# Kernel optimization log

Hardware: AMD Instinct MI355X
Metric: run time of the kernel (lower is better)

Reference implementation:

```python
import jax, jax.numpy as jnp
import numpy as np

B, S, E, NH = 2, 2048, 512, 4
DH = E // NH  # 128
KSZ = 4      # causal conv kernel size


def setup_inputs() -> dict:
    key = jax.random.key(0)
    ks = jax.random.split(key, 12)
    hw_std = (2.0 / 5.0 / DH) ** 0.5
    return {
        "x": jax.random.normal(ks[0], (B, S, E), jnp.float32),
        "W_up": jax.random.normal(ks[1], (2 * E, E), jnp.float32) * 0.02,
        "Wq": jax.random.normal(ks[2], (NH, DH, DH), jnp.float32) * hw_std,
        "Wk": jax.random.normal(ks[3], (NH, DH, DH), jnp.float32) * hw_std,
        "Wv": jax.random.normal(ks[4], (NH, DH, DH), jnp.float32) * hw_std,
        "conv_w": jax.random.normal(ks[5], (E, E, KSZ), jnp.float32) * (1.0 / (E * KSZ) ** 0.5),
        "conv_b": jnp.zeros((E,), jnp.float32),
        "Wi": jax.random.normal(ks[6], (NH, 3 * E), jnp.float32) * 0.01,
        "bi": jax.random.normal(ks[7], (NH,), jnp.float32) * 0.1,
        "Wf": jax.random.normal(ks[8], (NH, 3 * E), jnp.float32) * 0.01,
        "bf": jax.random.normal(ks[9], (NH,), jnp.float32),
        "skip": jnp.ones((E,), jnp.float32),
        "W_down": jax.random.normal(ks[10], (E, E), jnp.float32) * 0.02,
        "b_down": jnp.zeros((E,), jnp.float32),
    }


def _headwise(u, W):
    # LinearHeadwiseExpand: x -> [B,S,NH,dh] @ [NH,od,dh]
    b, s, e = u.shape
    nh = W.shape[0]
    uh = u.reshape(b, s, nh, -1)
    return jnp.einsum('bshd,hod->bsho', uh, W).reshape(b, s, e)


def reference(x, W_up, Wq, Wk, Wv, conv_w, conv_b, Wi, bi, Wf, bf, skip, W_down, b_down):
    b, s, e = x.shape
    nh = Wq.shape[0]
    dh = e // nh
    eps = 1e-6

    x_inner = x @ W_up.T                        # [B,S,2E]
    x_mlstm, z = jnp.split(x_inner, 2, axis=-1)

    # causal conv1d: left-pad kernel_size-1, trim implicit via padding spec
    xc = jnp.transpose(x_mlstm, (0, 2, 1))      # [B,E,S]
    conv = jax.lax.conv_general_dilated(
        xc, conv_w, window_strides=(1,), padding=[(KSZ - 1, 0)],
        dimension_numbers=('NCH', 'OIH', 'NCH')) + conv_b[None, :, None]
    x_conv_act = jax.nn.silu(jnp.transpose(conv, (0, 2, 1)))  # [B,S,E]

    q = _headwise(x_conv_act, Wq)
    k = _headwise(x_conv_act, Wk)
    v = _headwise(x_mlstm, Wv)

    gate_in = jnp.concatenate([q, k, v], axis=-1)           # [B,S,3E]
    igate = jnp.transpose(gate_in @ Wi.T + bi, (0, 2, 1))   # [B,NH,S]
    fgate = jnp.transpose(gate_in @ Wf.T + bf, (0, 2, 1))   # [B,NH,S]

    qh = jnp.transpose(q.reshape(b, s, nh, dh), (0, 2, 1, 3))  # [B,NH,S,DH]
    kh = jnp.transpose(k.reshape(b, s, nh, dh), (0, 2, 1, 3))
    vh = jnp.transpose(v.reshape(b, s, nh, dh), (0, 2, 1, 3))

    # log-space cumulative forget-gate D matrix
    log_fg = jax.nn.log_sigmoid(fgate)                      # [B,NH,S]
    lfc = jnp.cumsum(log_fg, axis=-1)                       # [B,NH,S]
    log_fg_mat = lfc[..., :, None] - lfc[..., None, :]      # [B,NH,S,S]
    mask = jnp.tril(jnp.ones((s, s), bool))
    log_fg_mat = jnp.where(mask, log_fg_mat, -jnp.inf)
    log_D = log_fg_mat + igate[..., None, :]                # + igate[j]

    max_log_D = jnp.max(log_D, axis=-1, keepdims=True)      # rowwise stabilize
    Dm = jnp.exp(log_D - max_log_D)

    qk = jnp.einsum('bhsd,bhtd->bhst', qh, kh) / (dh ** 0.5)
    C = qk * Dm
    normalizer = jnp.maximum(jnp.abs(jnp.sum(C, axis=-1, keepdims=True)),
                             jnp.exp(-max_log_D))
    Cn = C / (normalizer + eps)
    h = jnp.einsum('bhst,bhtd->bhsd', Cn, vh)               # [B,NH,S,DH]

    # MultiHeadLayerNorm = group_norm(num_groups=NH, no affine, eps=1e-5)
    ht = jnp.transpose(h, (0, 2, 1, 3))                     # [B,S,NH,DH]
    mean = jnp.mean(ht, axis=-1, keepdims=True)
    var = jnp.var(ht, axis=-1, keepdims=True)
    h_norm = ((ht - mean) / jnp.sqrt(var + 1e-5)).reshape(b, s, e)

    h_skip = h_norm + skip * x_conv_act
    h_state = h_skip * jax.nn.silu(z)
    return h_state @ W_down.T + b_down
```

## Files before the change

kernel.cpp:

```cpp
#include <hip/hip_runtime.h>
#include <hip/hip_bf16.h>
#include <math.h>

typedef __hip_bfloat16 bf16;
typedef unsigned short ushort_t;
typedef __bf16 v8bf __attribute__((ext_vector_type(8)));
typedef float v4f __attribute__((ext_vector_type(4)));

#define B_   2
#define S_   2048
#define E_   512
#define NH_  4
#define DH_  128
#define NIN_ 14
#define NSPLIT_ 4

__device__ inline ushort_t f2bf(float f) {
  union { float f; unsigned u; } v; v.f = f;
  unsigned r = (v.u + 0x7FFFu + ((v.u >> 16) & 1u)) >> 16;
  return (ushort_t)r;
}
__device__ inline float bf2f(ushort_t u) {
  union { unsigned uu; float ff; } c; c.uu = (unsigned)u << 16; return c.ff;
}

struct CvtArgs {
  const void* src[NIN_];
  float* dst[NIN_];
  ushort_t* bdst[NIN_];
  int sz[NIN_];
};

__global__ __launch_bounds__(256) void convert_all(CvtArgs a, const unsigned* modew) {
  const bool isbf = (*modew == 0x3F803F80u);
  const int t = blockIdx.y;
  const int n = a.sz[t];
  const int base = blockIdx.x * 1024 + threadIdx.x;
  const float* sf = (const float*)a.src[t];
  const bf16*  sb = (const bf16*)a.src[t];
  const ushort_t* su = (const ushort_t*)a.src[t];
  float* d = a.dst[t];
  ushort_t* bd = a.bdst[t];
#pragma unroll
  for (int k = 0; k < 4; ++k) {
    int idx = base + k * 256;
    if (idx < n) {
      float f = isbf ? __bfloat162float(sb[idx]) : sf[idx];
      if (d)  d[idx] = f;
      if (bd) bd[idx] = isbf ? su[idx] : f2bf(f);
    }
  }
}

__global__ __launch_bounds__(256) void conv_repack(
    const void* __restrict__ src, ushort_t* __restrict__ Wt, const unsigned* __restrict__ modew)
{
  const bool isbf = (*modew == 0x3F803F80u);
  int idx = blockIdx.x * 256 + threadIdx.x;
  if (idx < E_ * E_ * 4) {
    int k = idx & 3, i = (idx >> 2) & (E_ - 1), o = idx >> 11;
    ushort_t v;
    if (isbf) v = ((const ushort_t*)src)[idx];
    else      v = f2bf(((const float*)src)[idx]);
    Wt[((size_t)k * E_ + o) * E_ + i] = v;
  }
}

__global__ __launch_bounds__(256) void gates_repack(
    const void* __restrict__ wi, const void* __restrict__ wf,
    ushort_t* __restrict__ Wgh, ushort_t* __restrict__ Wgl,
    const unsigned* __restrict__ modew)
{
  const bool isbf = (*modew == 0x3F803F80u);
  int idx = blockIdx.x * 256 + threadIdx.x;
  if (idx < 16 * 3 * E_) {
    int row = idx / (3 * E_), col = idx % (3 * E_);
    float w = 0.f;
    if (row < 4)      w = isbf ? bf2f(((const ushort_t*)wi)[row * 3 * E_ + col])
                               : ((const float*)wi)[row * 3 * E_ + col];
    else if (row < 8) w = isbf ? bf2f(((const ushort_t*)wf)[(row - 4) * 3 * E_ + col])
                               : ((const float*)wf)[(row - 4) * 3 * E_ + col];
    ushort_t hi = f2bf(w);
    Wgh[idx] = hi;
    Wgl[idx] = f2bf(w - bf2f(hi));
  }
}

template <bool HAS_BIAS, bool OUT_BF16, bool OUT_LO, bool OUT_DUAL>
__global__ __launch_bounds__(256, 4) void gemm_lds(
    const ushort_t* __restrict__ A,
    const ushort_t* __restrict__ Bm,
    const float* __restrict__ bias,
    ushort_t* __restrict__ Cb, ushort_t* __restrict__ Cl,
    void* __restrict__ Cd, int ldc,
    const unsigned* __restrict__ modew)
{
  const int m0 = (blockIdx.x & 63) << 6;
  const int n0 = (blockIdx.x >> 6) << 6;
  const int tid = threadIdx.x;
  const int wv = tid >> 6;
  const int lane = tid & 63;
  const int ln15 = lane & 15, quad = lane >> 4;

  constexpr int LP = 132;
  __shared__ ushort_t Ab[64 * LP];

  int srow[8], scol[8];
#pragma unroll
  for (int j = 0; j < 8; ++j) {
    int idx = j * 256 + tid;
    srow[j] = idx >> 5;
    scol[j] = (idx & 31) << 2;
  }
  ushort4 sreg[8];
  auto stage_load = [&](int c) {
#pragma unroll
    for (int j = 0; j < 8; ++j)
      sreg[j] = *(const ushort4*)(A + (size_t)(m0 + srow[j]) * E_ + c * 128 + scol[j]);
  };
  auto stage_write = [&]() {
#pragma unroll
    for (int j = 0; j < 8; ++j)
      *(ushort4*)&Ab[srow[j] * LP + scol[j]] = sreg[j];
  };

  v4f acc[4];
#pragma unroll
  for (int i = 0; i < 4; ++i) acc[i] = (v4f){0, 0, 0, 0};

  v8bf breg[4];
  auto loadB = [&](int c) {
    const ushort_t* bw = Bm + (size_t)(n0 + wv * 16 + ln15) * E_ + c * 128 + quad * 8;
#pragma unroll
    for (int k0 = 0; k0 < 4; ++k0)
      breg[k0] = *(const v8bf*)(bw + k0 * 32);
  };
  auto compute = [&]() {
#pragma unroll
    for (int k0 = 0; k0 < 4; ++k0) {
#pragma unroll
      for (int rt = 0; rt < 4; ++rt) {
        v8bf a = *(const v8bf*)&Ab[(rt * 16 + ln15) * LP + k0 * 32 + quad * 8];
        acc[rt] = __builtin_amdgcn_mfma_f32_16x16x32_bf16(a, breg[k0], acc[rt], 0, 0, 0);
      }
    }
  };

  stage_load(0);
  stage_write();
  __syncthreads();
#pragma unroll
  for (int c = 0; c < 4; ++c) {
    if (c < 3) stage_load(c + 1);
    loadB(c);
    compute();
    if (c < 3) {
      __syncthreads();
      stage_write();
      __syncthreads();
    }
  }

  bool obf = false;
  if (OUT_DUAL) obf = (*modew == 0x3F803F80u);
  const int col = n0 + wv * 16 + ln15;
  float bv = 0.f;
  if (HAS_BIAS) bv = bias[col];
#pragma unroll
  for (int rt = 0; rt < 4; ++rt) {
#pragma unroll
    for (int rr = 0; rr < 4; ++rr) {
      const int row = m0 + rt * 16 + quad * 4 + rr;
      float c = acc[rt][rr] + bv;
      const size_t off = (size_t)row * ldc + col;
      if (OUT_BF16) {
        ushort_t hi = f2bf(c);
        Cb[off] = hi;
        if (OUT_LO) Cl[off] = f2bf(c - bf2f(hi));
      }
      if (OUT_DUAL) {
        if (obf) ((bf16*)Cd)[off] = __float2bfloat16(c);
        else     ((float*)Cd)[off] = c;
      }
    }
  }
}

__global__ __launch_bounds__(256, 2) void conv_lds2(
    const ushort_t* __restrict__ xhi,
    const ushort_t* __restrict__ xlo,
    const ushort_t* __restrict__ Wt,
    const float* __restrict__ cb,
    float* __restrict__ xca,
    ushort_t* __restrict__ xcab)
{
  const int m0 = (blockIdx.x & 63) << 6;
  const int n0 = (blockIdx.x >> 6) << 6;
  const int tid = threadIdx.x;
  const int wv = tid >> 6;
  const int lane = tid & 63;
  const int ln15 = lane & 15, quad = lane >> 4;
  const bool boundary = (m0 & (S_ - 1)) == 0;

  constexpr int LP = 132;
  __shared__ ushort_t Ab[2][68 * LP];

  int srow[17], scol[17], sstr[17];
#pragma unroll
  for (int j = 0; j < 17; ++j) {
    int idx = j * 256 + tid;
    sstr[j] = idx / 2176;
    int rem = idx - sstr[j] * 2176;
    srow[j] = rem >> 5;
    scol[j] = (rem & 31) << 2;
  }
  ushort4 sreg[17];
  auto stage_load = [&](int c) {
#pragma unroll
    for (int j = 0; j < 17; ++j) {
      const ushort_t* src = sstr[j] ? xlo : xhi;
      sreg[j] = *(const ushort4*)(src + (ptrdiff_t)(m0 - 4 + srow[j]) * (2 * E_)
                                  + c * 128 + scol[j]);
    }
    if (boundary) {
#pragma unroll
      for (int j = 0; j < 17; ++j)
        if (srow[j] < 4) sreg[j] = make_ushort4(0, 0, 0, 0);
    }
  };
  auto stage_write = [&]() {
#pragma unroll
    for (int j = 0; j < 17; ++j)
      *(ushort4*)&Ab[sstr[j]][srow[j] * LP + scol[j]] = sreg[j];
  };

  v4f acc[4];
#pragma unroll
  for (int i = 0; i < 4; ++i) acc[i] = (v4f){0, 0, 0, 0};

  v8bf breg[16];
  auto loadB = [&](int c) {
    const ushort_t* bw = Wt + (size_t)(n0 + wv * 16 + ln15) * E_ + c * 128 + quad * 8;
#pragma unroll
    for (int t = 0; t < 4; ++t)
#pragma unroll
      for (int k0 = 0; k0 < 4; ++k0)
        breg[t * 4 + k0] = *(const v8bf*)(bw + (size_t)t * E_ * E_ + k0 * 32);
  };
  auto compute = [&]() {
#pragma unroll
    for (int t = 0; t < 4; ++t) {
#pragma unroll
      for (int k0 = 0; k0 < 4; ++k0) {
#pragma unroll
        for (int rt = 0; rt < 4; ++rt) {
          const int ro = (rt * 16 + ln15 + t + 1) * LP + k0 * 32 + quad * 8;
          v8bf a1 = *(const v8bf*)&Ab[0][ro];
          v8bf a2 = *(const v8bf*)&Ab[1][ro];
          acc[rt] = __builtin_amdgcn_mfma_f32_16x16x32_bf16(a1, breg[t * 4 + k0], acc[rt], 0, 0, 0);
          acc[rt] = __builtin_amdgcn_mfma_f32_16x16x32_bf16(a2, breg[t * 4 + k0], acc[rt], 0, 0, 0);
        }
      }
    }
  };

  stage_load(0);
  stage_write();
  __syncthreads();
#pragma unroll
  for (int c = 0; c < 4; ++c) {
    if (c < 3) stage_load(c + 1);
    loadB(c);
    compute();
    if (c < 3) {
      __syncthreads();
      stage_write();
      __syncthreads();
    }
  }

  const int col = n0 + wv * 16 + ln15;
  const float cbv = cb[col];
#pragma unroll
  for (int rt = 0; rt < 4; ++rt) {
#pragma unroll
    for (int rr = 0; rr < 4; ++rr) {
      const int row = m0 + rt * 16 + quad * 4 + rr;
      float c = acc[rt][rr] + cbv;
      float r = c / (1.f + __expf(-c));
      const size_t off = (size_t)row * E_ + col;
      xca[off] = r;
      xcab[off] = f2bf(r);
    }
  }
}

__global__ __launch_bounds__(256) void qkv_mfma(
    const ushort_t* __restrict__ xcab,
    const ushort_t* __restrict__ xmb,
    const ushort_t* __restrict__ wqb, const ushort_t* __restrict__ wkb, const ushort_t* __restrict__ wvb,
    ushort_t* __restrict__ qb, ushort_t* __restrict__ kb, ushort_t* __restrict__ vb,
    ushort_t* __restrict__ vtb)
{
  const int type = blockIdx.y >> 2;
  const int h = blockIdx.y & 3;
  const int m0 = blockIdx.x << 6;
  const int tid = threadIdx.x;
  const int wv = tid >> 6, lane = tid & 63;
  const int ln15 = lane & 15, quad = lane >> 4;

  const ushort_t* Asrc = (type == 2) ? (xmb + h * DH_) : (xcab + h * DH_);
  const int lda = (type == 2) ? (2 * E_) : E_;
  const ushort_t* W = ((type == 0) ? wqb : (type == 1) ? wkb : wvb) + (size_t)h * DH_ * DH_;
  ushort_t* dst = (type == 0) ? qb : (type == 1) ? kb : vb;

  v4f acc[8];
#pragma unroll
  for (int i = 0; i < 8; ++i) acc[i] = (v4f){0.f, 0.f, 0.f, 0.f};

  const ushort_t* arow = Asrc + (size_t)(m0 + wv * 16 + ln15) * lda + quad * 8;
  const ushort_t* brow = W + (size_t)ln15 * DH_ + quad * 8;
#pragma unroll
  for (int c = 0; c < 4; ++c) {
    v8bf a = *(const v8bf*)(arow + c * 32);
#pragma unroll
    for (int nt = 0; nt < 8; ++nt) {
      v8bf b = *(const v8bf*)(brow + (size_t)nt * 16 * DH_ + c * 32);
      acc[nt] = __builtin_amdgcn_mfma_f32_16x16x32_bf16(a, b, acc[nt], 0, 0, 0);
    }
  }
  const int bb = m0 >> 11;
  const int s0 = (m0 & (S_ - 1)) + wv * 16 + quad * 4;
#pragma unroll
  for (int nt = 0; nt < 8; ++nt) {
    ushort_t pk[4];
#pragma unroll
    for (int rr = 0; rr < 4; ++rr) {
      int m = m0 + wv * 16 + quad * 4 + rr;
      int s = m & (S_ - 1);
      int n = nt * 16 + ln15;
      ushort_t u = f2bf(acc[nt][rr]);
      pk[rr] = u;
      dst[((size_t)(bb * NH_ + h) * S_ + s) * DH_ + n] = u;
    }
    if (type == 2) {
      *(ushort4*)&vtb[((size_t)(bb * NH_ + h) * DH_ + nt * 16 + ln15) * S_ + s0] =
          make_ushort4(pk[0], pk[1], pk[2], pk[3]);
    }
  }
}

__global__ __launch_bounds__(64) void gates_mfma(
    const ushort_t* __restrict__ qb, const ushort_t* __restrict__ kb, const ushort_t* __restrict__ vb,
    const ushort_t* __restrict__ Wgh, const ushort_t* __restrict__ Wgl,
    const float* __restrict__ bi, const float* __restrict__ bfp,
    float* __restrict__ ig, float* __restrict__ fgo)
{
  const int m0 = blockIdx.x << 4;
  const int lane = threadIdx.x;
  const int ln15 = lane & 15, quad = lane >> 4;
  const int m = m0 + ln15;
  const int b = m >> 11, s = m & (S_ - 1);
  const size_t base0 = ((size_t)(b * NH_) * S_ + s) * DH_;

  v4f acc = (v4f){0.f, 0.f, 0.f, 0.f};
  const ushort_t* wh = Wgh + (size_t)ln15 * (3 * E_) + quad * 8;
  const ushort_t* wl = Wgl + (size_t)ln15 * (3 * E_) + quad * 8;
#pragma unroll
  for (int kk = 0; kk < 48; ++kk) {
    const int kg = kk * 32 + quad * 8;
    const int type = kg >> 9;
    const int h = (kg >> 7) & 3;
    const int d = kg & 127;
    const ushort_t* src = (type == 0) ? qb : (type == 1) ? kb : vb;
    v8bf a = *(const v8bf*)(src + base0 + (size_t)h * S_ * DH_ + d);
    v8bf bh2 = *(const v8bf*)(wh + kk * 32);
    v8bf bl2 = *(const v8bf*)(wl + kk * 32);
    acc = __builtin_amdgcn_mfma_f32_16x16x32_bf16(a, bh2, acc, 0, 0, 0);
    acc = __builtin_amdgcn_mfma_f32_16x16x32_bf16(a, bl2, acc, 0, 0, 0);
  }
  if (ln15 < 8) {
#pragma unroll
    for (int r = 0; r < 4; ++r) {
      int mm = m0 + quad * 4 + r;
      int bb2 = mm >> 11, ss = mm & (S_ - 1);
      if (ln15 < 4) ig [((size_t)(bb2 * NH_ + ln15)) * S_ + ss]       = acc[r] + bi[ln15];
      else          fgo[((size_t)(bb2 * NH_ + (ln15 - 4))) * S_ + ss] = acc[r] + bfp[ln15 - 4];
    }
  }
}

__global__ __launch_bounds__(256) void gate_scan(
    const float* __restrict__ fgv, const float* __restrict__ igv,
    float* __restrict__ lfc, float* __restrict__ gout, float* __restrict__ Mout)
{
  const int bh = blockIdx.x;
  const int tid = threadIdx.x;
  const float* f = fgv + (size_t)bh * S_;
  const float* ii = igv + (size_t)bh * S_;
  __shared__ float sb[256];
  float loc[8];
  float run = 0.f;
#pragma unroll
  for (int j = 0; j < 8; ++j) {
    float x = f[tid * 8 + j];
    float ls = (x >= 0.f) ? -log1pf(expf(-x)) : (x - log1pf(expf(x)));
    run += ls; loc[j] = run;
  }
  sb[tid] = run; __syncthreads();
  for (int off = 1; off < 256; off <<= 1) {
    float t = (tid >= off) ? sb[tid - off] : 0.f;
    __syncthreads();
    sb[tid] += t;
    __syncthreads();
  }
  float pre = (tid > 0) ? sb[tid - 1] : 0.f;
  float lv[8], gl[8];
  float mrun = -INFINITY;
#pragma unroll
  for (int j = 0; j < 8; ++j) {
    lv[j] = pre + loc[j];
    lfc[(size_t)bh * S_ + tid * 8 + j] = lv[j];
    float gg = ii[tid * 8 + j] - lv[j];
    gout[(size_t)bh * S_ + tid * 8 + j] = gg;
    mrun = fmaxf(mrun, gg); gl[j] = mrun;
  }
  __syncthreads();
  sb[tid] = mrun; __syncthreads();
  for (int off = 1; off < 256; off <<= 1) {
    float t = (tid >= off) ? sb[tid - off] : -INFINITY;
    __syncthreads();
    sb[tid] = fmaxf(sb[tid], t);
    __syncthreads();
  }
  float mpre = (tid > 0) ? sb[tid - 1] : -INFINITY;
#pragma unroll
  for (int j = 0; j < 8; ++j)
    Mout[(size_t)bh * S_ + tid * 8 + j] = fmaxf(mpre, gl[j]);
}

__global__ __launch_bounds__(256, 2) void attn_split(
    const ushort_t* __restrict__ qb, const ushort_t* __restrict__ kb,
    const ushort_t* __restrict__ vtb,
    const float* __restrict__ gv, const float* __restrict__ Mv,
    float* __restrict__ pbuf,
    float* __restrict__ pcs)
{
  const int bh = blockIdx.x & 7;
  const int j = (blockIdx.x >> 3) & 15;
  const int chunk = blockIdx.x >> 7;
  const ushort_t* q = qb + (size_t)bh * S_ * DH_;
  const ushort_t* k = kb + (size_t)bh * S_ * DH_;
  const ushort_t* vt = vtb + (size_t)bh * DH_ * S_;
  const float* gp = gv + (size_t)bh * S_;
  const float* Mp = Mv + (size_t)bh * S_;

  __shared__ ushort_t Ps[4][2][16][72];

  const int tid = threadIdx.x;
  const int wv = tid >> 6;
  const int lane = tid & 63;
  const int ln15 = lane & 15;
  const int quad = lane >> 4;
  const int rowLo = (j * 4 + wv) * 16;
  const int rowHi = rowLo + 1024;
  const float lrs = 2.4245772f;

  ushort_t (*PsLo)[72] = Ps[wv][0];
  ushort_t (*PsHi)[72] = Ps[wv][1];

  v8bf qfL[4], qfH[4];
#pragma unroll
  for (int c = 0; c < 4; ++c) {
    qfL[c] = *(const v8bf*)(q + (size_t)(rowLo + ln15) * DH_ + c * 32 + quad * 8);
    qfH[c] = *(const v8bf*)(q + (size_t)(rowHi + ln15) * DH_ + c * 32 + quad * 8);
  }
  float MrL[4], MrH[4];
#pragma unroll
  for (int r = 0; r < 4; ++r) {
    MrL[r] = Mp[rowLo + quad * 4 + r] + lrs;
    MrH[r] = Mp[rowHi + quad * 4 + r] + lrs;
  }

  v4f haccL[8], haccH[8];
#pragma unroll
  for (int i = 0; i < 8; ++i) { haccL[i] = (v4f){0,0,0,0}; haccH[i] = (v4f){0,0,0,0}; }
  float csL[4] = {0,0,0,0}, csH[4] = {0,0,0,0};

  const int NI = 17 + j;
  const int it0 = (chunk * NI) / NSPLIT_;
  const int it1 = ((chunk + 1) * NI) / NSPLIT_;

  for (int it = it0; it < it1; ++it) {
    const int t0 = it << 6;
    const bool full2  = (t0 + 63 <= rowLo);
    const bool anyLo  = (t0 <= rowLo + 15);
    const bool fullHi = (t0 + 63 <= rowHi);

    if (full2) {
      v8bf kf[4][4];
#pragma unroll
      for (int tt = 0; tt < 4; ++tt) {
        const ushort_t* kr = k + (size_t)(t0 + tt * 16 + ln15) * DH_ + quad * 8;
#pragma unroll
        for (int c = 0; c < 4; ++c) kf[tt][c] = *(const v8bf*)(kr + c * 32);
      }
      v8bf vf0[8];
#pragma unroll
      for (int dt = 0; dt < 8; ++dt)
        vf0[dt] = *(const v8bf*)(vt + (size_t)(dt * 16 + ln15) * S_ + t0 + quad * 8);
#pragma unroll
      for (int tt = 0; tt < 4; ++tt) {
        v4f sL = (v4f){0,0,0,0}, sH = (v4f){0,0,0,0};
#pragma unroll
        for (int c = 0; c < 4; ++c) {
          sH = __builtin_amdgcn_mfma_f32_16x16x32_bf16(qfH[c], kf[tt][c], sH, 0, 0, 0);
          sL = __builtin_amdgcn_mfma_f32_16x16x32_bf16(qfL[c], kf[tt][c], sL, 0, 0, 0);
        }
        const float gt = gp[t0 + tt * 16 + ln15];
#pragma unroll
        for (int r = 0; r < 4; ++r) {
          float pH = sH[r] * __expf(fminf(gt - MrH[r], 60.f));
          float pL = sL[r] * __expf(fminf(gt - MrL[r], 60.f));
          csH[r] += pH; csL[r] += pL;
          PsHi[quad * 4 + r][tt * 16 + ln15] = f2bf(pH);
          PsLo[quad * 4 + r][tt * 16 + ln15] = f2bf(pL);
        }
      }
      {
        v8bf vf1[8];
#pragma unroll
        for (int dt = 0; dt < 8; ++dt)
          vf1[dt] = *(const v8bf*)(vt + (size_t)(dt * 16 + ln15) * S_ + t0 + 32 + quad * 8);
        v8bf pfH0 = *(const v8bf*)&PsHi[ln15][quad * 8];
        v8bf pfL0 = *(const v8bf*)&PsLo[ln15][quad * 8];
#pragma unroll
        for (int dt = 0; dt < 8; ++dt) {
          haccH[dt] = __builtin_amdgcn_mfma_f32_16x16x32_bf16(pfH0, vf0[dt], haccH[dt], 0, 0, 0);
          haccL[dt] = __builtin_amdgcn_mfma_f32_16x16x32_bf16(pfL0, vf0[dt], haccL[dt], 0, 0, 0);
        }
        v8bf pfH1 = *(const v8bf*)&PsHi[ln15][32 + quad * 8];
        v8bf pfL1 = *(const v8bf*)&PsLo[ln15][32 + quad * 8];
#pragma unroll
        for (int dt = 0; dt < 8; ++dt) {
          haccH[dt] = __builtin_amdgcn_mfma_f32_16x16x32_bf16(pfH1, vf1[dt], haccH[dt], 0, 0, 0);
          haccL[dt] = __builtin_amdgcn_mfma_f32_16x16x32_bf16(pfL1, vf1[dt], haccL[dt], 0, 0, 0);
        }
      }
    } else if (!anyLo && fullHi) {
      v8bf kf[4][4];
#pragma unroll
      for (int tt = 0; tt < 4; ++tt) {
        const ushort_t* kr = k + (size_t)(t0 + tt * 16 + ln15) * DH_ + quad * 8;
#pragma unroll
        for (int c = 0; c < 4; ++c) kf[tt][c] = *(const v8bf*)(kr + c * 32);
      }
      v8bf vf0[8];
#pragma unroll
      for (int dt = 0; dt < 8; ++dt)
        vf0[dt] = *(const v8bf*)(vt + (size_t)(dt * 16 + ln15) * S_ + t0 + quad * 8);
#pragma unroll
      for (int tt = 0; tt < 4; ++tt) {
        v4f sH = (v4f){0,0,0,0};
#pragma unroll
        for (int c = 0; c < 4; ++c)
          sH = __builtin_amdgcn_mfma_f32_16x16x32_bf16(qfH[c], kf[tt][c], sH, 0, 0, 0);
        const float gt = gp[t0 + tt * 16 + ln15];
#pragma unroll
        for (int r = 0; r < 4; ++r) {
          float pH = sH[r] * __expf(fminf(gt - MrH[r], 60.f));
          csH[r] += pH;
          PsHi[quad * 4 + r][tt * 16 + ln15] = f2bf(pH);
        }
      }
      {
        v8bf vf1[8];
#pragma unroll
        for (int dt = 0; dt < 8; ++dt)
          vf1[dt] = *(const v8bf*)(vt + (size_t)(dt * 16 + ln15) * S_ + t0 + 32 + quad * 8);
        v8bf pfH0 = *(const v8bf*)&PsHi[ln15][quad * 8];
#pragma unroll
        for (int dt = 0; dt < 8; ++dt)
          haccH[dt] = __builtin_amdgcn_mfma_f32_16x16x32_bf16(pfH0, vf0[dt], haccH[dt], 0, 0, 0);
        v8bf pfH1 = *(const v8bf*)&PsHi[ln15][32 + quad * 8];
#pragma unroll
        for (int dt = 0; dt < 8; ++dt)
          haccH[dt] = __builtin_amdgcn_mfma_f32_16x16x32_bf16(pfH1, vf1[dt], haccH[dt], 0, 0, 0);
      }
    } else {
      const bool loIter = anyLo;
#pragma unroll
      for (int tt = 0; tt < 4; ++tt) {
        const int tg0 = t0 + tt * 16;
        const bool hv = (tg0 <= rowHi + 15);
        const bool lv = (tg0 <= rowLo + 15);
        if (hv) {
          v4f sL = (v4f){0,0,0,0}, sH = (v4f){0,0,0,0};
          const ushort_t* kr = k + (size_t)(tg0 + ln15) * DH_ + quad * 8;
          if (lv) {
#pragma unroll
            for (int c = 0; c < 4; ++c) {
              v8bf kf = *(const v8bf*)(kr + c * 32);
              sH = __builtin_amdgcn_mfma_f32_16x16x32_bf16(qfH[c], kf, sH, 0, 0, 0);
              sL = __builtin_amdgcn_mfma_f32_16x16x32_bf16(qfL[c], kf, sL, 0, 0, 0);
            }
          } else {
#pragma unroll
            for (int c = 0; c < 4; ++c) {
              v8bf kf = *(const v8bf*)(kr + c * 32);
              sH = __builtin_amdgcn_mfma_f32_16x16x32_bf16(qfH[c], kf, sH, 0, 0, 0);
            }
          }
          const int tg = tg0 + ln15;
          const float gt = gp[tg];
#pragma unroll
          for (int r = 0; r < 4; ++r) {
            const int rowH = rowHi + quad * 4 + r;
            float p = sH[r] * __expf(fminf(gt - MrH[r], 60.f));
            p = (tg <= rowH) ? p : 0.f;
            csH[r] += p;
            PsHi[quad * 4 + r][tt * 16 + ln15] = f2bf(p);
          }
          if (lv) {
#pragma unroll
            for (int r = 0; r < 4; ++r) {
              const int rowL = rowLo + quad * 4 + r;
              float p = sL[r] * __expf(fminf(gt - MrL[r], 60.f));
              p = (tg <= rowL) ? p : 0.f;
              csL[r] += p;
              PsLo[quad * 4 + r][tt * 16 + ln15] = f2bf(p);
            }
          } else if (loIter) {
#pragma unroll
            for (int r = 0; r < 4; ++r) PsLo[quad * 4 + r][tt * 16 + ln15] = 0;
          }
        } else {
#pragma unroll
          for (int r = 0; r < 4; ++r) PsHi[quad * 4 + r][tt * 16 + ln15] = 0;
          if (loIter) {
#pragma unroll
            for (int r = 0; r < 4; ++r) PsLo[quad * 4 + r][tt * 16 + ln15] = 0;
          }
        }
      }
#pragma unroll
      for (int c2 = 0; c2 < 2; ++c2) {
        v8bf pfH = *(const v8bf*)&PsHi[ln15][c2 * 32 + quad * 8];
        if (loIter) {
          v8bf pfL = *(const v8bf*)&PsLo[ln15][c2 * 32 + quad * 8];
#pragma unroll
          for (int dt = 0; dt < 8; ++dt) {
            v8bf vf = *(const v8bf*)(vt + (size_t)(dt * 16 + ln15) * S_ + t0 + c2 * 32 + quad * 8);
            haccH[dt] = __builtin_amdgcn_mfma_f32_16x16x32_bf16(pfH, vf, haccH[dt], 0, 0, 0);
            haccL[dt] = __builtin_amdgcn_mfma_f32_16x16x32_bf16(pfL, vf, haccL[dt], 0, 0, 0);
          }
        } else {
#pragma unroll
          for (int dt = 0; dt < 8; ++dt) {
            v8bf vf = *(const v8bf*)(vt + (size_t)(dt * 16 + ln15) * S_ + t0 + c2 * 32 + quad * 8);
            haccH[dt] = __builtin_amdgcn_mfma_f32_16x16x32_bf16(pfH, vf, haccH[dt], 0, 0, 0);
          }
        }
      }
    }
  }

#pragma unroll
  for (int r = 0; r < 4; ++r) {
    float a = csL[r], b2 = csH[r];
    a += __shfl_xor(a, 1, 64);  b2 += __shfl_xor(b2, 1, 64);
    a += __shfl_xor(a, 2, 64);  b2 += __shfl_xor(b2, 2, 64);
    a += __shfl_xor(a, 4, 64);  b2 += __shfl_xor(b2, 4, 64);
    a += __shfl_xor(a, 8, 64);  b2 += __shfl_xor(b2, 8, 64);
    csL[r] = a; csH[r] = b2;
  }
  const size_t slab = (size_t)(chunk * 8 + bh);
  if (ln15 == 0) {
#pragma unroll
    for (int r = 0; r < 4; ++r) {
      __builtin_nontemporal_store(csL[r], &pcs[slab * S_ + rowLo + quad * 4 + r]);
      __builtin_nontemporal_store(csH[r], &pcs[slab * S_ + rowHi + quad * 4 + r]);
    }
  }
#pragma unroll
  for (int dt = 0; dt < 8; ++dt) {
#pragma unroll
    for (int r = 0; r < 4; ++r) {
      __builtin_nontemporal_store(haccL[dt][r],
          &pbuf[(slab * S_ + rowLo + quad * 4 + r) * DH_ + dt * 16 + ln15]);
      __builtin_nontemporal_store(haccH[dt][r],
          &pbuf[(slab * S_ + rowHi + quad * 4 + r) * DH_ + dt * 16 + ln15]);
    }
  }
}

__global__ __launch_bounds__(256) void gn_fused(
    const float* __restrict__ pbuf, const float* __restrict__ pcs,
    const float* __restrict__ Mv, const float* __restrict__ lfcv,
    const float* __restrict__ xca,
    const ushort_t* __restrict__ xhib, const ushort_t* __restrict__ xlob,
    const float* __restrict__ skip,
    ushort_t* __restrict__ hsb)
{
  const int row = blockIdx.x;
  const int b = row >> 11, s2 = row & (S_ - 1);
  const int tid = threadIdx.x;
  const int hd = tid >> 6, lane = tid & 63;
  const int bh = b * NH_ + hd;

  float v0 = 0.f, v1 = 0.f, cs = 0.f;
#pragma unroll
  for (int c = 0; c < NSPLIT_; ++c) {
    const size_t base = ((size_t)(c * 8 + bh) * S_ + s2) * DH_;
    v0 += __builtin_nontemporal_load(&pbuf[base + lane]);
    v1 += __builtin_nontemporal_load(&pbuf[base + lane + 64]);
    cs += __builtin_nontemporal_load(&pcs[(size_t)(c * 8 + bh) * S_ + s2]);
  }
  const size_t off = (size_t)bh * S_ + s2;
  const float floorv = __expf(fminf(-(lfcv[off] + Mv[off]), 80.f));
  const float inv = 1.f / (fmaxf(fabsf(cs), floorv) + 1e-6f);
  v0 *= inv; v1 *= inv;

  float s = v0 + v1, q = v0 * v0 + v1 * v1;
  for (int o = 32; o > 0; o >>= 1) { s += __shfl_down(s, o, 64); q += __shfl_down(q, o, 64); }
  s = __shfl(s, 0, 64); q = __shfl(q, 0, 64);
  float mean = s * (1.f / 128.f);
  float var = q * (1.f / 128.f) - mean * mean;
  float rstd = rsqrtf(fmaxf(var, 0.f) + 1e-5f);
#pragma unroll
  for (int t2 = 0; t2 < 2; ++t2) {
    int e = hd * DH_ + lane + t2 * 64;
    float hv = (t2 == 0) ? v0 : v1;
    float hn = (hv - mean) * rstd;
    float hs = hn + skip[e] * xca[(size_t)row * E_ + e];
    size_t zoff = (size_t)row * (2 * E_) + E_ + e;
    float z = bf2f(xhib[zoff]) + bf2f(xlob[zoff]);
    float sz = z / (1.f + __expf(-z));
    hsb[(size_t)row * E_ + e] = f2bf(hs * sz);
  }
}

extern "C" void kernel_launch(void* const* d_in, const int* in_sizes, int n_in,
                              void* d_out, int out_size, void* d_ws, size_t ws_size,
                              hipStream_t stream) {
  (void)out_size; (void)ws_size; (void)n_in;
  const unsigned* modew = (const unsigned*)d_in[11];

  float* ws = (float*)d_ws;
  size_t cur = 0;
  auto allocf = [&](size_t n) { float* p = ws + cur; cur += (n + 3) & ~(size_t)3; return p; };
  auto allocb = [&](size_t n) { return (ushort_t*)allocf((n + 1) / 2); };

  const bool needf[NIN_] = {false,false,false,false,false,false,true,false,true,false,true,true,false,true};
  const bool needb[NIN_] = {true,true,true,true,true,false,false,false,false,false,false,false,true,false};

  float* cvf[NIN_];
  ushort_t* cvb[NIN_];
  CvtArgs ca;
  int maxsz = 0;
  for (int i = 0; i < NIN_; ++i) {
    cvf[i] = needf[i] ? allocf((size_t)in_sizes[i]) : nullptr;
    cvb[i] = needb[i] ? allocb((size_t)in_sizes[i]) : nullptr;
    ca.src[i] = d_in[i];
    ca.dst[i] = cvf[i];
    ca.bdst[i] = cvb[i];
    ca.sz[i] = in_sizes[i];
    if (in_sizes[i] > maxsz) maxsz = in_sizes[i];
  }

  const size_t nBS = (size_t)B_ * S_;
  ushort_t* Wtc      = allocb((size_t)4 * E_ * E_);
  ushort_t* Wgh      = allocb((size_t)16 * 3 * E_);
  ushort_t* Wgl      = allocb((size_t)16 * 3 * E_);
  ushort_t* x_innerb = allocb(nBS * 2 * E_);
  ushort_t* x_lob    = allocb(nBS * 2 * E_);
  float* xca         = allocf(nBS * E_);
  ushort_t* xcab     = allocb(nBS * E_);
  ushort_t* qbuf     = allocb(nBS * E_);
  ushort_t* kbuf     = allocb(nBS * E_);
  ushort_t* vbuf     = allocb(nBS * E_);
  ushort_t* vtbuf    = allocb(nBS * E_);
  float* ig      = allocf((size_t)B_ * NH_ * S_);
  float* fg      = allocf((size_t)B_ * NH_ * S_);
  float* lfc     = allocf((size_t)B_ * NH_ * S_);
  float* gbuf    = allocf((size_t)B_ * NH_ * S_);
  float* Mbuf    = allocf((size_t)B_ * NH_ * S_);
  float* pbuf    = allocf((size_t)NSPLIT_ * 8 * S_ * DH_);
  float* pcs     = allocf((size_t)NSPLIT_ * 8 * S_);
  ushort_t* hsb  = allocb(nBS * E_);

  convert_all<<<dim3((maxsz + 1023) / 1024, NIN_), 256, 0, stream>>>(ca, modew);
  conv_repack<<<dim3((E_ * E_ * 4 + 255) / 256), 256, 0, stream>>>(d_in[5], Wtc, modew);
  gates_repack<<<dim3((16 * 3 * E_ + 255) / 256), 256, 0, stream>>>(d_in[7], d_in[9], Wgh, Wgl, modew);
  gemm_lds<false, true, true, false><<<dim3(64 * 16), 256, 0, stream>>>(
      cvb[0], cvb[1], nullptr, x_innerb, x_lob, nullptr, 2 * E_, modew);
  conv_lds2<<<dim3(64 * 8), 256, 0, stream>>>(x_innerb, x_lob, Wtc, cvf[6], xca, xcab);
  qkv_mfma<<<dim3(4096 / 64, 12), 256, 0, stream>>>(xcab, x_innerb, cvb[2], cvb[3], cvb[4],
                                                    qbuf, kbuf, vbuf, vtbuf);
  gates_mfma<<<dim3(4096 / 16), 64, 0, stream>>>(qbuf, kbuf, vbuf, Wgh, Wgl,
                                                 cvf[8], cvf[10], ig, fg);
  gate_scan<<<dim3(B_ * NH_), 256, 0, stream>>>(fg, ig, lfc, gbuf, Mbuf);
  attn_split<<<dim3(16 * NSPLIT_ * 8), 256, 0, stream>>>(
      qbuf, kbuf, vtbuf, gbuf, Mbuf, pbuf, pcs);
  gn_fused<<<dim3(4096), 256, 0, stream>>>(pbuf, pcs, Mbuf, lfc, xca, x_innerb, x_lob,
                                           cvf[11], hsb);
  gemm_lds<true, false, false, true><<<dim3(64 * 8), 256, 0, stream>>>(
      hsb, cvb[12], cvf[13], nullptr, nullptr, d_out, E_, modew);
}
```

Measured before the change: 264.5 us.

## Stage K/V tiles in shared memory with register prefetch of next tile

The attention split kernel now cooperatively loads each 64-row K tile and its V^T slice into padded shared memory, so the block loads them once instead of each of the four waves loading them directly from global memory. The next tile is prefetched into registers while the current one is computed, then written to LDS between two barriers. This cuts redundant global and L2 traffic, at the cost of extra LDS (about 34KB), more registers for the staging buffers, and two block barriers per iteration, which may lower occupancy below the two-blocks-per-CU launch bound.

```diff
diff --git a/kernel.cpp b/kernel.cpp
--- a/kernel.cpp
+++ b/kernel.cpp
@@ -455,7 +455,11 @@
   const float* gp = gv + (size_t)bh * S_;
   const float* Mp = Mv + (size_t)bh * S_;
 
+  constexpr int KP = 132;
+  constexpr int VP = 68;
   __shared__ ushort_t Ps[4][2][16][72];
+  __shared__ ushort_t Ks[64 * KP];
+  __shared__ ushort_t Vs[128 * VP];
 
   const int tid = threadIdx.x;
   const int wv = tid >> 6;
@@ -469,6 +473,29 @@
   ushort_t (*PsLo)[72] = Ps[wv][0];
   ushort_t (*PsHi)[72] = Ps[wv][1];
 
+  int krow[8], kcol[8], vrow[8], vcol[8];
+#pragma unroll
+  for (int i = 0; i < 8; ++i) {
+    int idx = i * 256 + tid;
+    krow[i] = idx >> 5;  kcol[i] = (idx & 31) << 2;
+    vrow[i] = idx >> 4;  vcol[i] = (idx & 15) << 2;
+  }
+  ushort4 ksr[8], vsr[8];
+  auto stage_load = [&](int t0) {
+#pragma unroll
+    for (int i = 0; i < 8; ++i) {
+      ksr[i] = *(const ushort4*)(k + (size_t)(t0 + krow[i]) * DH_ + kcol[i]);
+      vsr[i] = *(const ushort4*)(vt + (size_t)vrow[i] * S_ + t0 + vcol[i]);
+    }
+  };
+  auto stage_write = [&]() {
+#pragma unroll
+    for (int i = 0; i < 8; ++i) {
+      *(ushort4*)&Ks[krow[i] * KP + kcol[i]] = ksr[i];
+      *(ushort4*)&Vs[vrow[i] * VP + vcol[i]] = vsr[i];
+    }
+  };
+
   v8bf qfL[4], qfH[4];
 #pragma unroll
   for (int c = 0; c < 4; ++c) {
@@ -491,31 +518,29 @@
   const int it0 = (chunk * NI) / NSPLIT_;
   const int it1 = ((chunk + 1) * NI) / NSPLIT_;
 
+  stage_load(it0 << 6);
+  stage_write();
+  __syncthreads();
+
   for (int it = it0; it < it1; ++it) {
     const int t0 = it << 6;
+    const bool more = (it + 1 < it1);
+    if (more) stage_load((it + 1) << 6);
+
     const bool full2  = (t0 + 63 <= rowLo);
     const bool anyLo  = (t0 <= rowLo + 15);
     const bool fullHi = (t0 + 63 <= rowHi);
 
     if (full2) {
-      v8bf kf[4][4];
-#pragma unroll
-      for (int tt = 0; tt < 4; ++tt) {
-        const ushort_t* kr = k + (size_t)(t0 + tt * 16 + ln15) * DH_ + quad * 8;
-#pragma unroll
-        for (int c = 0; c < 4; ++c) kf[tt][c] = *(const v8bf*)(kr + c * 32);
-      }
-      v8bf vf0[8];
-#pragma unroll
-      for (int dt = 0; dt < 8; ++dt)
-        vf0[dt] = *(const v8bf*)(vt + (size_t)(dt * 16 + ln15) * S_ + t0 + quad * 8);
 #pragma unroll
       for (int tt = 0; tt < 4; ++tt) {
         v4f sL = (v4f){0,0,0,0}, sH = (v4f){0,0,0,0};
+        const ushort_t* kr = &Ks[(tt * 16 + ln15) * KP + quad * 8];
 #pragma unroll
         for (int c = 0; c < 4; ++c) {
-          sH = __builtin_amdgcn_mfma_f32_16x16x32_bf16(qfH[c], kf[tt][c], sH, 0, 0, 0);
-          sL = __builtin_amdgcn_mfma_f32_16x16x32_bf16(qfL[c], kf[tt][c], sL, 0, 0, 0);
+          v8bf kf = *(const v8bf*)(kr + c * 32);
+          sH = __builtin_amdgcn_mfma_f32_16x16x32_bf16(qfH[c], kf, sH, 0, 0, 0);
+          sL = __builtin_amdgcn_mfma_f32_16x16x32_bf16(qfL[c], kf, sL, 0, 0, 0);
         }
         const float gt = gp[t0 + tt * 16 + ln15];
 #pragma unroll
@@ -527,44 +552,27 @@
           PsLo[quad * 4 + r][tt * 16 + ln15] = f2bf(pL);
         }
       }
-      {
-        v8bf vf1[8];
-#pragma unroll
-        for (int dt = 0; dt < 8; ++dt)
-          vf1[dt] = *(const v8bf*)(vt + (size_t)(dt * 16 + ln15) * S_ + t0 + 32 + quad * 8);
-        v8bf pfH0 = *(const v8bf*)&PsHi[ln15][quad * 8];
-        v8bf pfL0 = *(const v8bf*)&PsLo[ln15][quad * 8];
+#pragma unroll
+      for (int c2 = 0; c2 < 2; ++c2) {
+        v8bf pfH = *(const v8bf*)&PsHi[ln15][c2 * 32 + quad * 8];
+        v8bf pfL = *(const v8bf*)&PsLo[ln15][c2 * 32 + quad * 8];
 #pragma unroll
         for (int dt = 0; dt < 8; ++dt) {
-          haccH[dt] = __builtin_amdgcn_mfma_f32_16x16x32_bf16(pfH0, vf0[dt], haccH[dt], 0, 0, 0);
-          haccL[dt] = __builtin_amdgcn_mfma_f32_16x16x32_bf16(pfL0, vf0[dt], haccL[dt], 0, 0, 0);
+          v8bf vf = *(const v8bf*)&Vs[(dt * 16 + ln15) * VP + c2 * 32 + quad * 8];
+          haccH[dt] = __builtin_amdgcn_mfma_f32_16x16x32_bf16(pfH, vf, haccH[dt], 0, 0, 0);
+          haccL[dt] = __builtin_amdgcn_mfma_f32_16x16x32_bf16(pfL, vf, haccL[dt], 0, 0, 0);
         }
-        v8bf pfH1 = *(const v8bf*)&PsHi[ln15][32 + quad * 8];
-        v8bf pfL1 = *(const v8bf*)&PsLo[ln15][32 + quad * 8];
-#pragma unroll
-        for (int dt = 0; dt < 8; ++dt) {
-          haccH[dt] = __builtin_amdgcn_mfma_f32_16x16x32_bf16(pfH1, vf1[dt], haccH[dt], 0, 0, 0);
-          haccL[dt] = __builtin_amdgcn_mfma_f32_16x16x32_bf16(pfL1, vf1[dt], haccL[dt], 0, 0, 0);
-        }
       }
     } else if (!anyLo && fullHi) {
-      v8bf kf[4][4];
-#pragma unroll
-      for (int tt = 0; tt < 4; ++tt) {
-        const ushort_t* kr = k + (size_t)(t0 + tt * 16 + ln15) * DH_ + quad * 8;
-#pragma unroll
-        for (int c = 0; c < 4; ++c) kf[tt][c] = *(const v8bf*)(kr + c * 32);
-      }
-      v8bf vf0[8];
-#pragma unroll
-      for (int dt = 0; dt < 8; ++dt)
-        vf0[dt] = *(const v8bf*)(vt + (size_t)(dt * 16 + ln15) * S_ + t0 + quad * 8);
 #pragma unroll
       for (int tt = 0; tt < 4; ++tt) {
         v4f sH = (v4f){0,0,0,0};
-#pragma unroll
-        for (int c = 0; c < 4; ++c)
-          sH = __builtin_amdgcn_mfma_f32_16x16x32_bf16(qfH[c], kf[tt][c], sH, 0, 0, 0);
+        const ushort_t* kr = &Ks[(tt * 16 + ln15) * KP + quad * 8];
+#pragma unroll
+        for (int c = 0; c < 4; ++c) {
+          v8bf kf = *(const v8bf*)(kr + c * 32);
+          sH = __builtin_amdgcn_mfma_f32_16x16x32_bf16(qfH[c], kf, sH, 0, 0, 0);
+        }
         const float gt = gp[t0 + tt * 16 + ln15];
 #pragma unroll
         for (int r = 0; r < 4; ++r) {
@@ -573,19 +581,14 @@
           PsHi[quad * 4 + r][tt * 16 + ln15] = f2bf(pH);
         }
       }
-      {
-        v8bf vf1[8];
-#pragma unroll
-        for (int dt = 0; dt < 8; ++dt)
-          vf1[dt] = *(const v8bf*)(vt + (size_t)(dt * 16 + ln15) * S_ + t0 + 32 + quad * 8);
-        v8bf pfH0 = *(const v8bf*)&PsHi[ln15][quad * 8];
-#pragma unroll
-        for (int dt = 0; dt < 8; ++dt)
-          haccH[dt] = __builtin_amdgcn_mfma_f32_16x16x32_bf16(pfH0, vf0[dt], haccH[dt], 0, 0, 0);
-        v8bf pfH1 = *(const v8bf*)&PsHi[ln15][32 + quad * 8];
-#pragma unroll
-        for (int dt = 0; dt < 8; ++dt)
-          haccH[dt] = __builtin_amdgcn_mfma_f32_16x16x32_bf16(pfH1, vf1[dt], haccH[dt], 0, 0, 0);
+#pragma unroll
+      for (int c2 = 0; c2 < 2; ++c2) {
+        v8bf pfH = *(const v8bf*)&PsHi[ln15][c2 * 32 + quad * 8];
+#pragma unroll
+        for (int dt = 0; dt < 8; ++dt) {
+          v8bf vf = *(const v8bf*)&Vs[(dt * 16 + ln15) * VP + c2 * 32 + quad * 8];
+          haccH[dt] = __builtin_amdgcn_mfma_f32_16x16x32_bf16(pfH, vf, haccH[dt], 0, 0, 0);
+        }
       }
     } else {
       const bool loIter = anyLo;
@@ -596,7 +599,7 @@
         const bool lv = (tg0 <= rowLo + 15);
         if (hv) {
           v4f sL = (v4f){0,0,0,0}, sH = (v4f){0,0,0,0};
-          const ushort_t* kr = k + (size_t)(tg0 + ln15) * DH_ + quad * 8;
+          const ushort_t* kr = &Ks[(tt * 16 + ln15) * KP + quad * 8];
           if (lv) {
 #pragma unroll
             for (int c = 0; c < 4; ++c) {
@@ -650,18 +653,24 @@
           v8bf pfL = *(const v8bf*)&PsLo[ln15][c2 * 32 + quad * 8];
 #pragma unroll
           for (int dt = 0; dt < 8; ++dt) {
-            v8bf vf = *(const v8bf*)(vt + (size_t)(dt * 16 + ln15) * S_ + t0 + c2 * 32 + quad * 8);
+            v8bf vf = *(const v8bf*)&Vs[(dt * 16 + ln15) * VP + c2 * 32 + quad * 8];
             haccH[dt] = __builtin_amdgcn_mfma_f32_16x16x32_bf16(pfH, vf, haccH[dt], 0, 0, 0);
             haccL[dt] = __builtin_amdgcn_mfma_f32_16x16x32_bf16(pfL, vf, haccL[dt], 0, 0, 0);
           }
         } else {
 #pragma unroll
           for (int dt = 0; dt < 8; ++dt) {
-            v8bf vf = *(const v8bf*)(vt + (size_t)(dt * 16 + ln15) * S_ + t0 + c2 * 32 + quad * 8);
+            v8bf vf = *(const v8bf*)&Vs[(dt * 16 + ln15) * VP + c2 * 32 + quad * 8];
             haccH[dt] = __builtin_amdgcn_mfma_f32_16x16x32_bf16(pfH, vf, haccH[dt], 0, 0, 0);
           }
         }
       }
+    }
+
+    if (more) {
+      __syncthreads();
+      stage_write();
+      __syncthreads();
     }
   }
 
```

Measured after the change: 267.5 us. No clear change (+1.1%).
